# Optimization experiments

Measured on AMD Instinct MI355X. Metric: run time of the kernel, lower is better.

## Reference

```python
import jax, jax.numpy as jnp
from jax import lax
import numpy as np

DIM = 800
FEAT = 192
LAYERS = 5
BLOCK_SZ = [32, 192, 192, 192, 192]
BLOCK_RNG = [0, 32, 224, 416, 608, 800]
HALF = 27  # image_size//4//2 - 1 with image_size=224
EPS = 1e-5


def conv2d(x, w, stride=1, pad=0, groups=1):
    return lax.conv_general_dilated(
        x, w, (stride, stride), [(pad, pad), (pad, pad)],
        dimension_numbers=("NCHW", "OIHW", "NCHW"),
        feature_group_count=groups)


def _bcast(v):
    return v[None, :, None, None]


def setup_inputs() -> dict:
    key = jax.random.key(0)
    ks = jax.random.split(key, 22)
    B = 32
    s = 0.05
    return {
        "x": jax.random.normal(ks[0], (B, 3, 224, 224), jnp.float32),
        "ds_w1": jax.random.normal(ks[1], (16, 3, 3, 3), jnp.float32) * s,
        "ds_b1": jax.random.normal(ks[2], (16,), jnp.float32) * s,
        "bn1_g": jax.random.uniform(ks[3], (16,), jnp.float32) + 0.5,
        "bn1_b": jax.random.normal(ks[4], (16,), jnp.float32) * s,
        "bn1_m": jax.random.normal(ks[5], (16,), jnp.float32) * s,
        "bn1_v": jax.random.uniform(ks[6], (16,), jnp.float32) + 0.5,
        "ds_dw": jax.random.normal(ks[7], (16, 1, 3, 3), jnp.float32) * s,
        "ds_dwb": jax.random.normal(ks[8], (16,), jnp.float32) * s,
        "ds_w2": jax.random.normal(ks[9], (32, 16, 1, 1), jnp.float32) * s,
        "ds_b2": jax.random.normal(ks[10], (32,), jnp.float32) * s,
        "bn2_g": jax.random.uniform(ks[11], (32,), jnp.float32) + 0.5,
        "bn2_b": jax.random.normal(ks[12], (32,), jnp.float32) * s,
        "bn2_m": jax.random.normal(ks[13], (32,), jnp.float32) * s,
        "bn2_v": jax.random.uniform(ks[14], (32,), jnp.float32) + 0.5,
        "conv_dw": jax.random.normal(ks[15], (DIM, 1, 3, 3), jnp.float32) * s,
        "gw": jax.random.normal(ks[16], (DIM, DIM), jnp.float32) * s,
        "in_gamma": jax.random.uniform(ks[17], (DIM,), jnp.float32) + 0.5,
        "in_beta": jax.random.normal(ks[18], (DIM,), jnp.float32) * s,
        "fc_w": jax.random.normal(ks[19], (1000, FEAT), jnp.float32) * s,
        "fc_b": jax.random.normal(ks[20], (1000,), jnp.float32) * s,
    }


def _forward(x, ds_w1, ds_b1, bn1_g, bn1_b, bn1_m, bn1_v, ds_dw, ds_dwb,
             ds_w2, ds_b2, bn2_g, bn2_b, bn2_m, bn2_v, conv_dw, gw,
             in_gamma, in_beta, fc_w, fc_b):
    # ---- downsample stem: conv3x3 s2 -> BN -> ReLU -> dwconv3x3 s2 -> conv1x1 -> BN
    h = conv2d(x, ds_w1, 2, 1) + _bcast(ds_b1)
    h = (h - _bcast(bn1_m)) * _bcast(bn1_g * lax.rsqrt(bn1_v + EPS)) + _bcast(bn1_b)
    h = jax.nn.relu(h)
    h = conv2d(h, ds_dw, 2, 1, groups=16) + _bcast(ds_dwb)
    h = conv2d(h, ds_w2, 1, 0) + _bcast(ds_b2)
    h = (h - _bcast(bn2_m)) * _bcast(bn2_g * lax.rsqrt(bn2_v + EPS)) + _bcast(bn2_b)
    B, _, H, W = h.shape  # (B, 32, 56, 56)
    h = jnp.concatenate([h, jnp.zeros((B, DIM - 32, H, W), h.dtype)], axis=1)

    # ---- per-block InstanceNorm -> ReLU -> depthwise conv -> sliced 1x1 graph conv -> residual
    for i in range(LAYERS):
        s, r0, r1 = BLOCK_SZ[i], BLOCK_RNG[i], BLOCK_RNG[i + 1]
        xa = h[:, :s]
        mu = xa.mean((2, 3), keepdims=True)
        var = ((xa - mu) ** 2).mean((2, 3), keepdims=True)
        xa = (xa - mu) * lax.rsqrt(var + EPS)
        xa = xa * _bcast(in_gamma[r0:r1]) + _bcast(in_beta[r0:r1])
        xa = jax.nn.relu(xa)
        xa = conv2d(xa, conv_dw[r0:r1], 1, 1, groups=s)
        row0 = min(r1, DIM - FEAT)
        xa = jnp.einsum("oc,bchw->bohw", gw[row0:, r0:r1], xa)
        h = (h[:, s:] if i < LAYERS - 1 else h[:, -FEAT:]) + xa

    # ---- AvgPool2d(2) over the 3x3 crop keeps only the top-left 2x2 mean
    out = h[:, :, HALF - 1:HALF + 1, HALF - 1:HALF + 1].mean((2, 3))
    return out @ fc_w.T + fc_b


def reference(x, ds_w1, ds_b1, bn1_g, bn1_b, bn1_m, bn1_v, ds_dw, ds_dwb,
              ds_w2, ds_b2, bn2_g, bn2_b, bn2_m, bn2_v, conv_dw, gw,
              in_gamma, in_beta, fc_w, fc_b):
    return _forward(x, ds_w1, ds_b1, bn1_g, bn1_b, bn1_m, bn1_v, ds_dw, ds_dwb,
                    ds_w2, ds_b2, bn2_g, bn2_b, bn2_m, bn2_v, conv_dw, gw,
                    in_gamma, in_beta, fc_w, fc_b)
```

## Files before the change

### kernel.cpp

```cpp
#include <hip/hip_runtime.h>
#include <stddef.h>

#define EPS 1e-5f
#define N_HW 3136
#define G 32
#define NG (G * N_HW)
#define DIMC 800
#define NTILE 49

typedef unsigned short u16;
typedef __attribute__((ext_vector_type(8))) short short8;
typedef __attribute__((ext_vector_type(4))) float floatx4;

__device__ __forceinline__ u16 f2b(float f) {
  unsigned u = __float_as_uint(f);
  u += 0x7FFFu + ((u >> 16) & 1u);
  return (u16)(u >> 16);
}
__device__ __forceinline__ float blo(unsigned u) { return __uint_as_float(u << 16); }
__device__ __forceinline__ float bhi(unsigned u) { return __uint_as_float(u & 0xFFFF0000u); }

static const size_t XA_OFF  = 0;
static const size_t H0_OFF  = 122028032ull;
static const size_t BLK_OFF = 134873088ull;
static const size_t GWB_OFF = 173408256ull;
static const size_t STS_OFF = 174688256ull;
static const size_t STQ_OFF = 174712832ull;
static const size_t PAT_OFF = 174737408ull;
static const size_t M4_OFF  = 179456000ull;
static const size_t MH_OFF  = M4_OFF + 6144 * 4;
static const size_t OP_OFF  = MH_OFF + 6144 * 4;
static const size_t NEED    = OP_OFF + 6144 * 4;

__global__ __launch_bounds__(256) void gw2bf(const float* __restrict__ gw, u16* __restrict__ gwb) {
  int i = (blockIdx.x * 256 + threadIdx.x) * 4;
  float4 v = *(const float4*)(gw + i);
  gwb[i + 0] = f2b(v.x); gwb[i + 1] = f2b(v.y);
  gwb[i + 2] = f2b(v.z); gwb[i + 3] = f2b(v.w);
}

__global__ __launch_bounds__(256) void zero_stats(float* __restrict__ p) {
  p[blockIdx.x * 256 + threadIdx.x] = 0.f;
}

#define XT_PITCH 226
#define XT_CH (17 * XT_PITCH)
__global__ __launch_bounds__(256) void stem_conv1(
    const float* __restrict__ xg, const float* __restrict__ w, const float* __restrict__ b1,
    const float* __restrict__ g, const float* __restrict__ bb,
    const float* __restrict__ m, const float* __restrict__ v,
    float* __restrict__ h1) {
  __shared__ float xt[3 * XT_CH];
  __shared__ float wt[16 * 27];
  __shared__ float mulc[16], addc[16];
  int blk = blockIdx.x;
  int s = blk % 14;
  int bg = blk / 14;
  int tid = threadIdx.x;

  for (int e = tid; e < 432; e += 256) wt[e] = w[e];
  if (tid < 16) {
    float A = g[tid] * rsqrtf(v[tid] + EPS);
    mulc[tid] = A;
    addc[tid] = (b1[tid] - m[tid]) * A + bb[tid];
  }
  int iy0 = 16 * s - 1;
  for (int e = tid; e < 3 * XT_CH; e += 256) {
    int ci = e / XT_CH;
    int rem = e - ci * XT_CH;
    int r = rem / XT_PITCH;
    int cc = rem - r * XT_PITCH;
    int iy = iy0 + r, ix = cc - 1;
    float val = 0.f;
    if (iy >= 0 && iy < 224 && ix >= 0 && ix < 224)
      val = xg[((size_t)(bg * 3 + ci)) * 224 * 224 + iy * 224 + ix];
    xt[e] = val;
  }
  __syncthreads();

  for (int p = tid; p < 8 * 112; p += 256) {
    int oyl = p / 112, ox = p - oyl * 112;
    float xv[27];
#pragma unroll
    for (int ci = 0; ci < 3; ci++)
#pragma unroll
      for (int ky = 0; ky < 3; ky++)
#pragma unroll
        for (int kx = 0; kx < 3; kx++)
          xv[ci * 9 + ky * 3 + kx] = xt[ci * XT_CH + (2 * oyl + ky) * XT_PITCH + 2 * ox + kx];
    int oy = 8 * s + oyl;
#pragma unroll
    for (int c = 0; c < 16; c++) {
      float acc = 0.f;
#pragma unroll
      for (int t = 0; t < 27; t++) acc += xv[t] * wt[c * 27 + t];
      float y = acc * mulc[c] + addc[c];
      h1[(size_t)(c * G + bg) * 12544 + oy * 112 + ox] = fmaxf(y, 0.f);
    }
  }
}

__global__ __launch_bounds__(256) void stem_dw(
    const float* __restrict__ h1, const float* __restrict__ dw, const float* __restrict__ dwb,
    float* __restrict__ h2) {
  int idx = blockIdx.x * 256 + threadIdx.x;
  int q = idx % N_HW;
  int t = idx / N_HW;
  int bg = t & (G - 1);
  int c = t >> 5;
  int qy = q / 56, qx = q % 56;
  const float* plane = h1 + (size_t)(c * G + bg) * 12544;
  float acc = dwb[c];
#pragma unroll
  for (int ky = 0; ky < 3; ky++) {
    int iy = qy * 2 - 1 + ky;
    if (iy < 0 || iy >= 112) continue;
#pragma unroll
    for (int kx = 0; kx < 3; kx++) {
      int ix = qx * 2 - 1 + kx;
      if (ix < 0 || ix >= 112) continue;
      acc += plane[iy * 112 + ix] * dw[c * 9 + ky * 3 + kx];
    }
  }
  h2[idx] = acc;
}

__global__ __launch_bounds__(256) void stem_pw(
    const float* __restrict__ h2, const float* __restrict__ w2, const float* __restrict__ b2,
    const float* __restrict__ g, const float* __restrict__ bb,
    const float* __restrict__ m, const float* __restrict__ v,
    float* __restrict__ H0) {
  int idx = blockIdx.x * 256 + threadIdx.x;
  int q = idx % N_HW;
  int t = idx / N_HW;
  int bg = t & (G - 1);
  int o = t >> 5;
  float acc = b2[o];
#pragma unroll
  for (int c = 0; c < 16; c++) acc += w2[o * 16 + c] * h2[(size_t)(c * G + bg) * N_HW + q];
  float y = (acc - m[o]) * (g[o] * rsqrtf(v[o] + EPS)) + bb[o];
  H0[idx] = y;
}

template <typename T>
__global__ __launch_bounds__(256) void dw_fused(
    const T* __restrict__ base, const float* __restrict__ cdw,
    const float* __restrict__ in_g, const float* __restrict__ in_b,
    u16* __restrict__ XA, int cdwoff) {
  __shared__ float sm[58 * 58];
  __shared__ float wred[8];
  int blk = blockIdx.x;
  int cl = blk >> 5;
  int c = cdwoff + cl;
  int tid = threadIdx.x;

  if (tid < 58) { sm[tid] = 0.f; sm[57 * 58 + tid] = 0.f; }
  if (tid >= 64 && tid < 120) { int r = tid - 63; sm[r * 58] = 0.f; sm[r * 58 + 57] = 0.f; }

  const T* row = base + (size_t)blk * N_HW;
  float s = 0.f, s2 = 0.f;
  for (int i = tid; i < 392; i += 256) {
    float vals[8];
    if constexpr (sizeof(T) == 2) {
      uint4 u = *(const uint4*)((const u16*)row + i * 8);
      vals[0] = blo(u.x); vals[1] = bhi(u.x);
      vals[2] = blo(u.y); vals[3] = bhi(u.y);
      vals[4] = blo(u.z); vals[5] = bhi(u.z);
      vals[6] = blo(u.w); vals[7] = bhi(u.w);
    } else {
      float4 v0 = *(const float4*)((const float*)row + i * 8);
      float4 v1 = *(const float4*)((const float*)row + i * 8 + 4);
      vals[0] = v0.x; vals[1] = v0.y; vals[2] = v0.z; vals[3] = v0.w;
      vals[4] = v1.x; vals[5] = v1.y; vals[6] = v1.z; vals[7] = v1.w;
    }
    int p = i * 8;
    int y = p / 56, x = p - y * 56;
    float* d = &sm[(y + 1) * 58 + x + 1];
#pragma unroll
    for (int e = 0; e < 8; e++) {
      d[e] = vals[e];
      s += vals[e];
      s2 += vals[e] * vals[e];
    }
  }
#pragma unroll
  for (int o = 32; o > 0; o >>= 1) {
    s += __shfl_down(s, o);
    s2 += __shfl_down(s2, o);
  }
  if ((tid & 63) == 0) { wred[(tid >> 6) * 2] = s; wred[(tid >> 6) * 2 + 1] = s2; }
  __syncthreads();
  float ts = (wred[0] + wred[2]) + (wred[4] + wred[6]);
  float tq = (wred[1] + wred[3]) + (wred[5] + wred[7]);
  float mean = ts * (1.f / N_HW);
  float var = fmaxf(tq * (1.f / N_HW) - mean * mean, 0.f);
  float sc = in_g[c] * rsqrtf(var + EPS);
  float sh = in_b[c] - mean * sc;

  for (int i = tid; i < N_HW; i += 256) {
    int y = i / 56, x = i - y * 56;
    int pos = (y + 1) * 58 + x + 1;
    sm[pos] = fmaxf(sm[pos] * sc + sh, 0.f);
  }
  __syncthreads();

  float w0 = cdw[c * 9 + 0], w1 = cdw[c * 9 + 1], w2 = cdw[c * 9 + 2];
  float w3 = cdw[c * 9 + 3], w4 = cdw[c * 9 + 4], w5 = cdw[c * 9 + 5];
  float w6 = cdw[c * 9 + 6], w7 = cdw[c * 9 + 7], w8 = cdw[c * 9 + 8];
  u16* outp = XA + (size_t)blk * N_HW;
  for (int pp = tid; pp < N_HW / 2; pp += 256) {
    int p = pp * 2;
    int y = p / 56, x = p - y * 56;
    const float* p0 = &sm[y * 58 + x];
    float a0 = p0[0] * w0 + p0[1] * w1 + p0[2] * w2
             + p0[58] * w3 + p0[59] * w4 + p0[60] * w5
             + p0[116] * w6 + p0[117] * w7 + p0[118] * w8;
    float a1 = p0[1] * w0 + p0[2] * w1 + p0[3] * w2
             + p0[59] * w3 + p0[60] * w4 + p0[61] * w5
             + p0[117] * w6 + p0[118] * w7 + p0[119] * w8;
    unsigned pk = (unsigned)f2b(a0) | ((unsigned)f2b(a1) << 16);
    *(unsigned*)&outp[p] = pk;
  }
}

template <int MODE>
__global__ __launch_bounds__(256) void gemm_mfma(
    const u16* __restrict__ A, const u16* __restrict__ B, u16* __restrict__ C,
    float* __restrict__ statS, float* __restrict__ statQ, float* __restrict__ patchf,
    int K) {
  __shared__ u16 As[192][40];
  int n0 = blockIdx.x * 64;
  int tid = threadIdx.x;
  int wave = tid >> 6, lane = tid & 63;
  int wm = wave >> 1, wn = wave & 1;
  int lg = lane >> 4, li = lane & 15;
  floatx4 acc[6][2] = {};

  int ar = tid >> 2, ak = (tid & 3) * 8;
  const u16* Ag = A + (size_t)ar * DIMC + ak;
  const u16* Bg = B + (size_t)(lg * 8) * NG + n0 + wn * 32 + li;

  int nt = K / 32;
  uint4 ra0 = *(const uint4*)(Ag);
  uint4 ra1 = *(const uint4*)(Ag + (size_t)64 * DIMC);
  uint4 ra2 = *(const uint4*)(Ag + (size_t)128 * DIMC);
  short8 bF0, bF1;
#pragma unroll
  for (int e = 0; e < 8; e++) {
    bF0[e] = (short)Bg[(size_t)e * NG];
    bF1[e] = (short)Bg[(size_t)e * NG + 16];
  }

  for (int t = 0; t < nt; t++) {
    *(uint4*)&As[ar][ak]       = ra0;
    *(uint4*)&As[ar + 64][ak]  = ra1;
    *(uint4*)&As[ar + 128][ak] = ra2;
    __syncthreads();
    short8 nb0, nb1;
    bool pf = (t + 1 < nt);
    if (pf) {
      const u16* ag = Ag + (size_t)(t + 1) * 32;
      ra0 = *(const uint4*)(ag);
      ra1 = *(const uint4*)(ag + (size_t)64 * DIMC);
      ra2 = *(const uint4*)(ag + (size_t)128 * DIMC);
      const u16* bg = Bg + (size_t)(t + 1) * 32 * NG;
#pragma unroll
      for (int e = 0; e < 8; e++) {
        nb0[e] = (short)bg[(size_t)e * NG];
        nb1[e] = (short)bg[(size_t)e * NG + 16];
      }
    }
    short8 aF[6];
#pragma unroll
    for (int mi = 0; mi < 6; mi++)
      aF[mi] = *(const short8*)&As[wm * 96 + mi * 16 + li][lg * 8];
#pragma unroll
    for (int mi = 0; mi < 6; mi++) {
      acc[mi][0] = __builtin_amdgcn_mfma_f32_16x16x32_bf16(aF[mi], bF0, acc[mi][0], 0, 0, 0);
      acc[mi][1] = __builtin_amdgcn_mfma_f32_16x16x32_bf16(aF[mi], bF1, acc[mi][1], 0, 0, 0);
    }
    __syncthreads();
    if (pf) { bF0 = nb0; bF1 = nb1; }
  }

  if constexpr (MODE == 0) {
#pragma unroll
    for (int mi = 0; mi < 6; mi++) {
#pragma unroll
      for (int ni = 0; ni < 2; ni++) {
        int row = wm * 96 + mi * 16 + lg * 4;
        int col = n0 + wn * 32 + ni * 16 + li;
        u16* cp = C + (size_t)row * NG + col;
#pragma unroll
        for (int r = 0; r < 4; r++) cp[(size_t)r * NG] = f2b(acc[mi][ni][r]);
      }
    }
  } else {
    int bg = blockIdx.x / NTILE;
    int tile = blockIdx.x % NTILE;
#pragma unroll
    for (int mi = 0; mi < 6; mi++) {
#pragma unroll
      for (int r = 0; r < 4; r++) {
        float v0 = acc[mi][0][r], v1 = acc[mi][1][r];
        float s = v0 + v1;
        float q = v0 * v0 + v1 * v1;
#pragma unroll
        for (int msk = 1; msk < 16; msk <<= 1) {
          s += __shfl_xor(s, msk);
          q += __shfl_xor(q, msk);
        }
        if (li == 0) {
          int row = wm * 96 + mi * 16 + lg * 4 + r;
          atomicAdd(&statS[row * 32 + bg], s);
          atomicAdd(&statQ[row * 32 + bg], q);
        }
      }
    }
    if (tile >= 22 && tile <= 24) {
#pragma unroll
      for (int mi = 0; mi < 6; mi++) {
#pragma unroll
        for (int ni = 0; ni < 2; ni++) {
          int row = wm * 96 + mi * 16 + lg * 4;
          int pc = (tile - 22) * 64 + wn * 32 + ni * 16 + li;
#pragma unroll
          for (int r = 0; r < 4; r++)
            patchf[((size_t)(row + r) * 32 + bg) * 192 + pc] = acc[mi][ni][r];
        }
      }
    }
  }
}

__global__ __launch_bounds__(256) void head_m4(
    const float* __restrict__ statS, const float* __restrict__ statQ,
    const float* __restrict__ patchf,
    const float* __restrict__ in_g, const float* __restrict__ in_b,
    const float* __restrict__ cdw, float* __restrict__ m4, float* __restrict__ meanH) {
  int idx = blockIdx.x * 256 + threadIdx.x;
  if (idx >= 192 * 32) return;
  int cl = idx >> 5;
  int c = 608 + cl;
  float mean = statS[idx] * (1.f / N_HW);
  float var = fmaxf(statQ[idx] * (1.f / N_HW) - mean * mean, 0.f);
  float sc = in_g[c] * rsqrtf(var + EPS);
  float sh = in_b[c] - mean * sc;
  const float* pf = patchf + (size_t)idx * 192;
  float val[4][4];
#pragma unroll
  for (int dy = 0; dy < 4; dy++)
#pragma unroll
    for (int dx = 0; dx < 4; dx++) {
      int hw = (25 + dy) * 56 + 25 + dx;
      float v = pf[((hw >> 6) - 22) * 64 + (hw & 63)];
      val[dy][dx] = fmaxf(v * sc + sh, 0.f);
    }
  const float* w = cdw + c * 9;
  float acc = 0.f;
#pragma unroll
  for (int oy = 1; oy < 3; oy++)
#pragma unroll
    for (int ox = 1; ox < 3; ox++)
#pragma unroll
      for (int ky = 0; ky < 3; ky++)
#pragma unroll
        for (int kx = 0; kx < 3; kx++)
          acc += val[oy + ky - 1][ox + kx - 1] * w[ky * 3 + kx];
  m4[idx] = acc * 0.25f;
  float mh = 0.f;
#pragma unroll
  for (int dy = 0; dy < 2; dy++)
#pragma unroll
    for (int dx = 0; dx < 2; dx++) {
      int hw = (26 + dy) * 56 + 26 + dx;
      mh += pf[((hw >> 6) - 22) * 64 + (hw & 63)];
    }
  meanH[idx] = mh * 0.25f;
}

__global__ __launch_bounds__(256) void head_mix(
    const float* __restrict__ gw, const float* __restrict__ m4, const float* __restrict__ meanH,
    float* __restrict__ out_pre) {
  int idx = blockIdx.x * 256 + threadIdx.x;
  if (idx >= G * 192) return;
  int j = idx % 192;
  int bg = idx / 192;
  float acc = meanH[j * G + bg];
  const float* grow = gw + (size_t)(608 + j) * DIMC + 608;
  for (int c = 0; c < 192; c++) acc += grow[c] * m4[c * G + bg];
  out_pre[idx] = acc;
}

__global__ __launch_bounds__(256) void head_fc(
    const float* __restrict__ out_pre, const float* __restrict__ fc_w,
    const float* __restrict__ fc_b, float* __restrict__ outg) {
  int idx = blockIdx.x * 256 + threadIdx.x;
  if (idx >= G * 1000) return;
  int t = idx % 1000;
  int bg = idx / 1000;
  float acc = fc_b[t];
  const float* wr = fc_w + (size_t)t * 192;
  const float* hr = out_pre + (size_t)bg * 192;
  for (int j = 0; j < 192; j++) acc += wr[j] * hr[j];
  outg[idx] = acc;
}

extern "C" void kernel_launch(void* const* d_in, const int* in_sizes, int n_in,
                              void* d_out, int out_size, void* d_ws, size_t ws_size,
                              hipStream_t stream) {
  const float* x      = (const float*)d_in[0];
  const float* ds_w1  = (const float*)d_in[1];
  const float* ds_b1  = (const float*)d_in[2];
  const float* bn1_g  = (const float*)d_in[3];
  const float* bn1_b  = (const float*)d_in[4];
  const float* bn1_m  = (const float*)d_in[5];
  const float* bn1_v  = (const float*)d_in[6];
  const float* ds_dw  = (const float*)d_in[7];
  const float* ds_dwb = (const float*)d_in[8];
  const float* ds_w2  = (const float*)d_in[9];
  const float* ds_b2  = (const float*)d_in[10];
  const float* bn2_g  = (const float*)d_in[11];
  const float* bn2_b  = (const float*)d_in[12];
  const float* bn2_m  = (const float*)d_in[13];
  const float* bn2_v  = (const float*)d_in[14];
  const float* cdw    = (const float*)d_in[15];
  const float* gw     = (const float*)d_in[16];
  const float* in_g   = (const float*)d_in[17];
  const float* in_b   = (const float*)d_in[18];
  const float* fc_w   = (const float*)d_in[19];
  const float* fc_b   = (const float*)d_in[20];
  float* out = (float*)d_out;
  char* ws = (char*)d_ws;

  if (ws_size < NEED) return;

  u16*   XAc    = (u16*)(ws + XA_OFF);
  float* H0     = (float*)(ws + H0_OFF);
  u16*   blockb = (u16*)(ws + BLK_OFF);
  u16*   gwb    = (u16*)(ws + GWB_OFF);
  float* statS  = (float*)(ws + STS_OFF);
  float* statQ  = (float*)(ws + STQ_OFF);
  float* patchf = (float*)(ws + PAT_OFF);
  float* m4     = (float*)(ws + M4_OFF);
  float* meanH  = (float*)(ws + MH_OFF);
  float* opre   = (float*)(ws + OP_OFF);
  float* h1     = (float*)(ws + BLK_OFF);
  float* h2     = h1 + (size_t)16 * G * 12544;

  gw2bf<<<625, 256, 0, stream>>>(gw, gwb);
  zero_stats<<<48, 256, 0, stream>>>(statS);

  static const int CDWOFF[4] = {0, 32, 224, 416};
  static const int SZ[4]     = {32, 192, 192, 192};
  static const int RA[4]     = {32, 224, 416, 608};
  static const int KK[4]     = {32, 224, 416, 608};

  stem_conv1<<<14 * G, 256, 0, stream>>>(
      x, ds_w1, ds_b1, bn1_g, bn1_b, bn1_m, bn1_v, h1);
  stem_dw<<<16 * G * N_HW / 256, 256, 0, stream>>>(h1, ds_dw, ds_dwb, h2);
  stem_pw<<<32 * G * N_HW / 256, 256, 0, stream>>>(
      h2, ds_w2, ds_b2, bn2_g, bn2_b, bn2_m, bn2_v, H0);

  for (int i = 0; i < 4; i++) {
    if (i == 0)
      dw_fused<float><<<SZ[i] * G, 256, 0, stream>>>(
          H0, cdw, in_g, in_b, XAc + (size_t)CDWOFF[i] * NG, CDWOFF[i]);
    else
      dw_fused<u16><<<SZ[i] * G, 256, 0, stream>>>(
          blockb, cdw, in_g, in_b, XAc + (size_t)CDWOFF[i] * NG, CDWOFF[i]);
    if (i < 3)
      gemm_mfma<0><<<NG / 64, 256, 0, stream>>>(
          gwb + (size_t)RA[i] * DIMC, XAc, blockb, nullptr, nullptr, nullptr, KK[i]);
    else
      gemm_mfma<1><<<NG / 64, 256, 0, stream>>>(
          gwb + (size_t)RA[i] * DIMC, XAc, nullptr, statS, statQ, patchf, KK[i]);
  }

  head_m4<<<24, 256, 0, stream>>>(statS, statQ, patchf, in_g, in_b, cdw, m4, meanH);
  head_mix<<<(G * 192 + 255) / 256, 256, 0, stream>>>(gw, m4, meanH, opre);
  head_fc<<<(G * 1000 + 255) / 256, 256, 0, stream>>>(opre, fc_w, fc_b, out);
}
```

Baseline: 431.5 us.

## Store depthwise output in K-tiled layout and fuse instance-norm stats into producers

The depthwise kernel now writes its bf16 output in a K-tiled layout (32 channels contiguous per pixel), so the GEMM can load B fragments with two 16-byte loads instead of eight strided scalar loads. Instance-norm statistics are now accumulated with atomics in the producing kernels (stem pointwise and every GEMM epilogue). This lets the depthwise kernel work on 4-row strips across 32 channels instead of staging a full plane per channel. The head patch is also shrunk to the 4x4 pixels it needs. The cost is more atomics in every GEMM epilogue and a strided transposed store pattern in the depthwise kernel.

Result: slower. 699.6 us (+62.1%).

```diff
diff --git a/kernel.cpp b/kernel.cpp
--- a/kernel.cpp
+++ b/kernel.cpp
@@ -20,17 +20,16 @@
 __device__ __forceinline__ float blo(unsigned u) { return __uint_as_float(u << 16); }
 __device__ __forceinline__ float bhi(unsigned u) { return __uint_as_float(u & 0xFFFF0000u); }
 
-static const size_t XA_OFF  = 0;
-static const size_t H0_OFF  = 122028032ull;
-static const size_t BLK_OFF = 134873088ull;
-static const size_t GWB_OFF = 173408256ull;
-static const size_t STS_OFF = 174688256ull;
-static const size_t STQ_OFF = 174712832ull;
-static const size_t PAT_OFF = 174737408ull;
-static const size_t M4_OFF  = 179456000ull;
-static const size_t MH_OFF  = M4_OFF + 6144 * 4;
-static const size_t OP_OFF  = MH_OFF + 6144 * 4;
-static const size_t NEED    = OP_OFF + 6144 * 4;
+static const size_t XAKT_OFF = 0;
+static const size_t BUF1_OFF = 122028032ull;
+static const size_t H0F_OFF  = 160563200ull;
+static const size_t GWB_OFF  = 173408256ull;
+static const size_t STAT_OFF = 174688256ull;
+static const size_t P16_OFF  = 174934016ull;
+static const size_t M4_OFF   = 175327232ull;
+static const size_t MH_OFF   = M4_OFF + 6144 * 4;
+static const size_t OP_OFF   = MH_OFF + 6144 * 4;
+static const size_t NEED     = OP_OFF + 6144 * 4;
 
 __global__ __launch_bounds__(256) void gw2bf(const float* __restrict__ gw, u16* __restrict__ gwb) {
   int i = (blockIdx.x * 256 + threadIdx.x) * 4;
@@ -125,109 +124,136 @@
   h2[idx] = acc;
 }
 
-__global__ __launch_bounds__(256) void stem_pw(
+__global__ __launch_bounds__(256) void stem_pw_v2(
     const float* __restrict__ h2, const float* __restrict__ w2, const float* __restrict__ b2,
     const float* __restrict__ g, const float* __restrict__ bb,
     const float* __restrict__ m, const float* __restrict__ v,
-    float* __restrict__ H0) {
-  int idx = blockIdx.x * 256 + threadIdx.x;
-  int q = idx % N_HW;
-  int t = idx / N_HW;
-  int bg = t & (G - 1);
-  int o = t >> 5;
-  float acc = b2[o];
-#pragma unroll
-  for (int c = 0; c < 16; c++) acc += w2[o * 16 + c] * h2[(size_t)(c * G + bg) * N_HW + q];
-  float y = (acc - m[o]) * (g[o] * rsqrtf(v[o] + EPS)) + bb[o];
-  H0[idx] = y;
+    float* __restrict__ H0, float* __restrict__ stat0) {
+  int r = blockIdx.x;
+  int o = r >> 5, bg = r & 31;
+  int tid = threadIdx.x;
+  float w[16];
+#pragma unroll
+  for (int c = 0; c < 16; c++) w[c] = w2[o * 16 + c];
+  float A = g[o] * rsqrtf(v[o] + EPS);
+  float mul = A, add = bb[o] - m[o] * A;
+  const float* h2r = h2 + (size_t)bg * N_HW;
+  float* outp = H0 + (size_t)r * N_HW;
+  float s = 0.f, s2 = 0.f;
+  for (int q = tid; q < N_HW; q += 256) {
+    float acc = b2[o];
+#pragma unroll
+    for (int c = 0; c < 16; c++) acc += w[c] * h2r[(size_t)c * G * N_HW + q];
+    float y = acc * mul + add;
+    outp[q] = y;
+    s += y; s2 += y * y;
+  }
+#pragma unroll
+  for (int o2 = 32; o2 > 0; o2 >>= 1) {
+    s += __shfl_down(s, o2);
+    s2 += __shfl_down(s2, o2);
+  }
+  if ((tid & 63) == 0) {
+    atomicAdd(&stat0[r], s);
+    atomicAdd(&stat0[6144 + r], s2);
+  }
 }
 
 template <typename T>
-__global__ __launch_bounds__(256) void dw_fused(
-    const T* __restrict__ base, const float* __restrict__ cdw,
+__global__ __launch_bounds__(256) void dw_kt(
+    const T* __restrict__ in, const float* __restrict__ cdw,
     const float* __restrict__ in_g, const float* __restrict__ in_b,
-    u16* __restrict__ XA, int cdwoff) {
-  __shared__ float sm[58 * 58];
-  __shared__ float wred[8];
+    const float* __restrict__ stat, u16* __restrict__ XAkt,
+    int cdwoff, int ngroups) {
+  __shared__ float sm[32 * 350];
+  __shared__ float ssc[32], ssh[32], swt[32 * 9];
   int blk = blockIdx.x;
-  int cl = blk >> 5;
-  int c = cdwoff + cl;
+  int grp = blk % ngroups;
+  int t2 = blk / ngroups;
+  int strip = t2 % 14;
+  int bg = t2 / 14;
   int tid = threadIdx.x;
-
-  if (tid < 58) { sm[tid] = 0.f; sm[57 * 58 + tid] = 0.f; }
-  if (tid >= 64 && tid < 120) { int r = tid - 63; sm[r * 58] = 0.f; sm[r * 58 + 57] = 0.f; }
-
-  const T* row = base + (size_t)blk * N_HW;
-  float s = 0.f, s2 = 0.f;
-  for (int i = tid; i < 392; i += 256) {
-    float vals[8];
-    if constexpr (sizeof(T) == 2) {
-      uint4 u = *(const uint4*)((const u16*)row + i * 8);
-      vals[0] = blo(u.x); vals[1] = bhi(u.x);
-      vals[2] = blo(u.y); vals[3] = bhi(u.y);
-      vals[4] = blo(u.z); vals[5] = bhi(u.z);
-      vals[6] = blo(u.w); vals[7] = bhi(u.w);
+  if (tid < 32) {
+    int cl = grp * 32 + tid;
+    int c = cdwoff + cl;
+    int sidx = cl * 32 + bg;
+    float S = stat[sidx], Q = stat[6144 + sidx];
+    float mean = S * (1.f / N_HW);
+    float var = fmaxf(Q * (1.f / N_HW) - mean * mean, 0.f);
+    float sc = in_g[c] * rsqrtf(var + EPS);
+    ssc[tid] = sc;
+    ssh[tid] = in_b[c] - mean * sc;
+  }
+  for (int e = tid; e < 288; e += 256)
+    swt[e] = cdw[(size_t)(cdwoff + grp * 32) * 9 + e];
+  __syncthreads();
+
+  int y0 = strip * 4;
+  if (tid < 192) {
+    int ch = tid / 6, rr = tid % 6;
+    int y = y0 - 1 + rr;
+    float* dst = &sm[ch * 350 + rr * 58];
+    if (y < 0 || y > 55) {
+#pragma unroll
+      for (int x = 0; x < 58; x++) dst[x] = 0.f;
     } else {
-      float4 v0 = *(const float4*)((const float*)row + i * 8);
-      float4 v1 = *(const float4*)((const float*)row + i * 8 + 4);
-      vals[0] = v0.x; vals[1] = v0.y; vals[2] = v0.z; vals[3] = v0.w;
-      vals[4] = v1.x; vals[5] = v1.y; vals[6] = v1.z; vals[7] = v1.w;
-    }
-    int p = i * 8;
-    int y = p / 56, x = p - y * 56;
-    float* d = &sm[(y + 1) * 58 + x + 1];
-#pragma unroll
-    for (int e = 0; e < 8; e++) {
-      d[e] = vals[e];
-      s += vals[e];
-      s2 += vals[e] * vals[e];
-    }
-  }
-#pragma unroll
-  for (int o = 32; o > 0; o >>= 1) {
-    s += __shfl_down(s, o);
-    s2 += __shfl_down(s2, o);
-  }
-  if ((tid & 63) == 0) { wred[(tid >> 6) * 2] = s; wred[(tid >> 6) * 2 + 1] = s2; }
+      float sc = ssc[ch], sh = ssh[ch];
+      dst[0] = 0.f; dst[57] = 0.f;
+      const T* src = in + ((size_t)(grp * 32 + ch) * G + bg) * N_HW + y * 56;
+      if constexpr (sizeof(T) == 2) {
+#pragma unroll
+        for (int xx = 0; xx < 7; xx++) {
+          uint4 u = *(const uint4*)((const u16*)src + xx * 8);
+          float* d = dst + 1 + xx * 8;
+          d[0] = fmaxf(blo(u.x) * sc + sh, 0.f);
+          d[1] = fmaxf(bhi(u.x) * sc + sh, 0.f);
+          d[2] = fmaxf(blo(u.y) * sc + sh, 0.f);
+          d[3] = fmaxf(bhi(u.y) * sc + sh, 0.f);
+          d[4] = fmaxf(blo(u.z) * sc + sh, 0.f);
+          d[5] = fmaxf(bhi(u.z) * sc + sh, 0.f);
+          d[6] = fmaxf(blo(u.w) * sc + sh, 0.f);
+          d[7] = fmaxf(bhi(u.w) * sc + sh, 0.f);
+        }
+      } else {
+#pragma unroll
+        for (int xx = 0; xx < 14; xx++) {
+          float4 vv = *(const float4*)((const float*)src + xx * 4);
+          float* d = dst + 1 + xx * 4;
+          d[0] = fmaxf(vv.x * sc + sh, 0.f);
+          d[1] = fmaxf(vv.y * sc + sh, 0.f);
+          d[2] = fmaxf(vv.z * sc + sh, 0.f);
+          d[3] = fmaxf(vv.w * sc + sh, 0.f);
+        }
+      }
+    }
+  }
   __syncthreads();
-  float ts = (wred[0] + wred[2]) + (wred[4] + wred[6]);
-  float tq = (wred[1] + wred[3]) + (wred[5] + wred[7]);
-  float mean = ts * (1.f / N_HW);
-  float var = fmaxf(tq * (1.f / N_HW) - mean * mean, 0.f);
-  float sc = in_g[c] * rsqrtf(var + EPS);
-  float sh = in_b[c] - mean * sc;
-
-  for (int i = tid; i < N_HW; i += 256) {
-    int y = i / 56, x = i - y * 56;
-    int pos = (y + 1) * 58 + x + 1;
-    sm[pos] = fmaxf(sm[pos] * sc + sh, 0.f);
-  }
-  __syncthreads();
-
-  float w0 = cdw[c * 9 + 0], w1 = cdw[c * 9 + 1], w2 = cdw[c * 9 + 2];
-  float w3 = cdw[c * 9 + 3], w4 = cdw[c * 9 + 4], w5 = cdw[c * 9 + 5];
-  float w6 = cdw[c * 9 + 6], w7 = cdw[c * 9 + 7], w8 = cdw[c * 9 + 8];
-  u16* outp = XA + (size_t)blk * N_HW;
-  for (int pp = tid; pp < N_HW / 2; pp += 256) {
-    int p = pp * 2;
-    int y = p / 56, x = p - y * 56;
-    const float* p0 = &sm[y * 58 + x];
-    float a0 = p0[0] * w0 + p0[1] * w1 + p0[2] * w2
-             + p0[58] * w3 + p0[59] * w4 + p0[60] * w5
-             + p0[116] * w6 + p0[117] * w7 + p0[118] * w8;
-    float a1 = p0[1] * w0 + p0[2] * w1 + p0[3] * w2
-             + p0[59] * w3 + p0[60] * w4 + p0[61] * w5
-             + p0[117] * w6 + p0[118] * w7 + p0[119] * w8;
-    unsigned pk = (unsigned)f2b(a0) | ((unsigned)f2b(a1) << 16);
-    *(unsigned*)&outp[p] = pk;
+
+  size_t tilebase = ((size_t)(cdwoff >> 5) + grp) * NG;
+  for (int e = tid; e < 896; e += 256) {
+    int pos = e >> 2, k8 = e & 3;
+    int ry = pos / 56, x = pos % 56;
+    int y = y0 + ry;
+    u16 outv[8];
+#pragma unroll
+    for (int j = 0; j < 8; j++) {
+      int ch = k8 * 8 + j;
+      const float* b = &sm[ch * 350 + ry * 58 + x];
+      const float* w = &swt[ch * 9];
+      float a = b[0] * w[0] + b[1] * w[1] + b[2] * w[2]
+              + b[58] * w[3] + b[59] * w[4] + b[60] * w[5]
+              + b[116] * w[6] + b[117] * w[7] + b[118] * w[8];
+      outv[j] = f2b(a);
+    }
+    *(uint4*)(XAkt + (tilebase + (size_t)bg * N_HW + y * 56 + x) * 32 + k8 * 8) =
+        *(const uint4*)outv;
   }
 }
 
 template <int MODE>
-__global__ __launch_bounds__(256) void gemm_mfma(
-    const u16* __restrict__ A, const u16* __restrict__ B, u16* __restrict__ C,
-    float* __restrict__ statS, float* __restrict__ statQ, float* __restrict__ patchf,
-    int K) {
+__global__ __launch_bounds__(256) void gemm_v2(
+    const u16* __restrict__ A, const u16* __restrict__ Bkt, u16* __restrict__ C,
+    float* __restrict__ stat, float* __restrict__ p16, int K) {
   __shared__ u16 As[192][40];
   int n0 = blockIdx.x * 64;
   int tid = threadIdx.x;
@@ -238,51 +264,66 @@
 
   int ar = tid >> 2, ak = (tid & 3) * 8;
   const u16* Ag = A + (size_t)ar * DIMC + ak;
-  const u16* Bg = B + (size_t)(lg * 8) * NG + n0 + wn * 32 + li;
+  const u16* Bg = Bkt + ((size_t)(n0 + wn * 32 + li)) * 32 + lg * 8;
 
   int nt = K / 32;
   uint4 ra0 = *(const uint4*)(Ag);
   uint4 ra1 = *(const uint4*)(Ag + (size_t)64 * DIMC);
   uint4 ra2 = *(const uint4*)(Ag + (size_t)128 * DIMC);
-  short8 bF0, bF1;
-#pragma unroll
-  for (int e = 0; e < 8; e++) {
-    bF0[e] = (short)Bg[(size_t)e * NG];
-    bF1[e] = (short)Bg[(size_t)e * NG + 16];
-  }
+  uint4 rb0 = *(const uint4*)(Bg);
+  uint4 rb1 = *(const uint4*)(Bg + 512);
 
   for (int t = 0; t < nt; t++) {
     *(uint4*)&As[ar][ak]       = ra0;
     *(uint4*)&As[ar + 64][ak]  = ra1;
     *(uint4*)&As[ar + 128][ak] = ra2;
     __syncthreads();
-    short8 nb0, nb1;
+    uint4 nb0, nb1;
     bool pf = (t + 1 < nt);
     if (pf) {
       const u16* ag = Ag + (size_t)(t + 1) * 32;
       ra0 = *(const uint4*)(ag);
       ra1 = *(const uint4*)(ag + (size_t)64 * DIMC);
       ra2 = *(const uint4*)(ag + (size_t)128 * DIMC);
-      const u16* bg = Bg + (size_t)(t + 1) * 32 * NG;
-#pragma unroll
-      for (int e = 0; e < 8; e++) {
-        nb0[e] = (short)bg[(size_t)e * NG];
-        nb1[e] = (short)bg[(size_t)e * NG + 16];
-      }
+      const u16* bgp = Bg + (size_t)(t + 1) * NG * 32;
+      nb0 = *(const uint4*)(bgp);
+      nb1 = *(const uint4*)(bgp + 512);
     }
     short8 aF[6];
 #pragma unroll
     for (int mi = 0; mi < 6; mi++)
       aF[mi] = *(const short8*)&As[wm * 96 + mi * 16 + li][lg * 8];
+    short8 bF0 = *(short8*)&rb0;
+    short8 bF1 = *(short8*)&rb1;
 #pragma unroll
     for (int mi = 0; mi < 6; mi++) {
       acc[mi][0] = __builtin_amdgcn_mfma_f32_16x16x32_bf16(aF[mi], bF0, acc[mi][0], 0, 0, 0);
       acc[mi][1] = __builtin_amdgcn_mfma_f32_16x16x32_bf16(aF[mi], bF1, acc[mi][1], 0, 0, 0);
     }
     __syncthreads();
-    if (pf) { bF0 = nb0; bF1 = nb1; }
-  }
-
+    if (pf) { rb0 = nb0; rb1 = nb1; }
+  }
+
+  int bg = blockIdx.x / NTILE;
+#pragma unroll
+  for (int mi = 0; mi < 6; mi++) {
+#pragma unroll
+    for (int r = 0; r < 4; r++) {
+      float v0 = acc[mi][0][r], v1 = acc[mi][1][r];
+      float s = v0 + v1;
+      float q = v0 * v0 + v1 * v1;
+#pragma unroll
+      for (int msk = 1; msk < 16; msk <<= 1) {
+        s += __shfl_xor(s, msk);
+        q += __shfl_xor(q, msk);
+      }
+      if (li == 0) {
+        int row = wm * 96 + mi * 16 + lg * 4 + r;
+        atomicAdd(&stat[row * 32 + bg], s);
+        atomicAdd(&stat[6144 + row * 32 + bg], q);
+      }
+    }
+  }
   if constexpr (MODE == 0) {
 #pragma unroll
     for (int mi = 0; mi < 6; mi++) {
@@ -296,66 +337,45 @@
       }
     }
   } else {
-    int bg = blockIdx.x / NTILE;
-    int tile = blockIdx.x % NTILE;
-#pragma unroll
-    for (int mi = 0; mi < 6; mi++) {
-#pragma unroll
-      for (int r = 0; r < 4; r++) {
-        float v0 = acc[mi][0][r], v1 = acc[mi][1][r];
-        float s = v0 + v1;
-        float q = v0 * v0 + v1 * v1;
-#pragma unroll
-        for (int msk = 1; msk < 16; msk <<= 1) {
-          s += __shfl_xor(s, msk);
-          q += __shfl_xor(q, msk);
-        }
-        if (li == 0) {
-          int row = wm * 96 + mi * 16 + lg * 4 + r;
-          atomicAdd(&statS[row * 32 + bg], s);
-          atomicAdd(&statQ[row * 32 + bg], q);
-        }
+#pragma unroll
+    for (int ni = 0; ni < 2; ni++) {
+      int col = n0 + wn * 32 + ni * 16 + li;
+      int hw = col % 3136;
+      int yy = hw / 56, xx = hw % 56;
+      int dy = yy - 25, dx = xx - 25;
+      if ((unsigned)dy < 4u && (unsigned)dx < 4u) {
+#pragma unroll
+        for (int mi = 0; mi < 6; mi++)
+#pragma unroll
+          for (int r = 0; r < 4; r++) {
+            int row = wm * 96 + mi * 16 + lg * 4 + r;
+            p16[((size_t)row * 32 + bg) * 16 + dy * 4 + dx] = acc[mi][ni][r];
+          }
       }
     }
-    if (tile >= 22 && tile <= 24) {
-#pragma unroll
-      for (int mi = 0; mi < 6; mi++) {
-#pragma unroll
-        for (int ni = 0; ni < 2; ni++) {
-          int row = wm * 96 + mi * 16 + lg * 4;
-          int pc = (tile - 22) * 64 + wn * 32 + ni * 16 + li;
-#pragma unroll
-          for (int r = 0; r < 4; r++)
-            patchf[((size_t)(row + r) * 32 + bg) * 192 + pc] = acc[mi][ni][r];
-        }
-      }
-    }
   }
 }
 
 __global__ __launch_bounds__(256) void head_m4(
-    const float* __restrict__ statS, const float* __restrict__ statQ,
-    const float* __restrict__ patchf,
+    const float* __restrict__ stat4, const float* __restrict__ p16,
     const float* __restrict__ in_g, const float* __restrict__ in_b,
     const float* __restrict__ cdw, float* __restrict__ m4, float* __restrict__ meanH) {
   int idx = blockIdx.x * 256 + threadIdx.x;
   if (idx >= 192 * 32) return;
   int cl = idx >> 5;
   int c = 608 + cl;
-  float mean = statS[idx] * (1.f / N_HW);
-  float var = fmaxf(statQ[idx] * (1.f / N_HW) - mean * mean, 0.f);
+  float S = stat4[idx], Q = stat4[6144 + idx];
+  float mean = S * (1.f / N_HW);
+  float var = fmaxf(Q * (1.f / N_HW) - mean * mean, 0.f);
   float sc = in_g[c] * rsqrtf(var + EPS);
   float sh = in_b[c] - mean * sc;
-  const float* pf = patchf + (size_t)idx * 192;
+  const float* pf = p16 + (size_t)idx * 16;
   float val[4][4];
 #pragma unroll
   for (int dy = 0; dy < 4; dy++)
 #pragma unroll
-    for (int dx = 0; dx < 4; dx++) {
-      int hw = (25 + dy) * 56 + 25 + dx;
-      float v = pf[((hw >> 6) - 22) * 64 + (hw & 63)];
-      val[dy][dx] = fmaxf(v * sc + sh, 0.f);
-    }
+    for (int dx = 0; dx < 4; dx++)
+      val[dy][dx] = fmaxf(pf[dy * 4 + dx] * sc + sh, 0.f);
   const float* w = cdw + c * 9;
   float acc = 0.f;
 #pragma unroll
@@ -368,15 +388,7 @@
         for (int kx = 0; kx < 3; kx++)
           acc += val[oy + ky - 1][ox + kx - 1] * w[ky * 3 + kx];
   m4[idx] = acc * 0.25f;
-  float mh = 0.f;
-#pragma unroll
-  for (int dy = 0; dy < 2; dy++)
-#pragma unroll
-    for (int dx = 0; dx < 2; dx++) {
-      int hw = (26 + dy) * 56 + 26 + dx;
-      mh += pf[((hw >> 6) - 22) * 64 + (hw & 63)];
-    }
-  meanH[idx] = mh * 0.25f;
+  meanH[idx] = 0.25f * (pf[5] + pf[6] + pf[9] + pf[10]);
 }
 
 __global__ __launch_bounds__(256) void head_mix(
@@ -435,49 +447,50 @@
 
   if (ws_size < NEED) return;
 
-  u16*   XAc    = (u16*)(ws + XA_OFF);
-  float* H0     = (float*)(ws + H0_OFF);
-  u16*   blockb = (u16*)(ws + BLK_OFF);
-  u16*   gwb    = (u16*)(ws + GWB_OFF);
-  float* statS  = (float*)(ws + STS_OFF);
-  float* statQ  = (float*)(ws + STQ_OFF);
-  float* patchf = (float*)(ws + PAT_OFF);
-  float* m4     = (float*)(ws + M4_OFF);
-  float* meanH  = (float*)(ws + MH_OFF);
-  float* opre   = (float*)(ws + OP_OFF);
-  float* h1     = (float*)(ws + BLK_OFF);
-  float* h2     = h1 + (size_t)16 * G * 12544;
+  u16*   XAkt  = (u16*)(ws + XAKT_OFF);
+  u16*   buf1  = (u16*)(ws + BUF1_OFF);
+  float* H0f   = (float*)(ws + H0F_OFF);
+  u16*   gwb   = (u16*)(ws + GWB_OFF);
+  float* stats = (float*)(ws + STAT_OFF);
+  float* p16   = (float*)(ws + P16_OFF);
+  float* m4    = (float*)(ws + M4_OFF);
+  float* meanH = (float*)(ws + MH_OFF);
+  float* opre  = (float*)(ws + OP_OFF);
+  float* h1    = (float*)buf1;
+  float* h2    = h1 + (size_t)16 * G * 12544;
 
   gw2bf<<<625, 256, 0, stream>>>(gw, gwb);
-  zero_stats<<<48, 256, 0, stream>>>(statS);
+  zero_stats<<<240, 256, 0, stream>>>(stats);
 
   static const int CDWOFF[4] = {0, 32, 224, 416};
-  static const int SZ[4]     = {32, 192, 192, 192};
+  static const int NGRP[4]   = {1, 6, 6, 6};
   static const int RA[4]     = {32, 224, 416, 608};
   static const int KK[4]     = {32, 224, 416, 608};
 
   stem_conv1<<<14 * G, 256, 0, stream>>>(
       x, ds_w1, ds_b1, bn1_g, bn1_b, bn1_m, bn1_v, h1);
   stem_dw<<<16 * G * N_HW / 256, 256, 0, stream>>>(h1, ds_dw, ds_dwb, h2);
-  stem_pw<<<32 * G * N_HW / 256, 256, 0, stream>>>(
-      h2, ds_w2, ds_b2, bn2_g, bn2_b, bn2_m, bn2_v, H0);
+  stem_pw_v2<<<1024, 256, 0, stream>>>(
+      h2, ds_w2, ds_b2, bn2_g, bn2_b, bn2_m, bn2_v, H0f, stats );
 
   for (int i = 0; i < 4; i++) {
+    float* statIn  = stats + (size_t)i * 12288;
+    float* statOut = stats + (size_t)(i + 1) * 12288;
     if (i == 0)
-      dw_fused<float><<<SZ[i] * G, 256, 0, stream>>>(
-          H0, cdw, in_g, in_b, XAc + (size_t)CDWOFF[i] * NG, CDWOFF[i]);
+      dw_kt<float><<<32 * 14 * NGRP[i], 256, 0, stream>>>(
+          H0f, cdw, in_g, in_b, statIn, XAkt, CDWOFF[i], NGRP[i]);
     else
-      dw_fused<u16><<<SZ[i] * G, 256, 0, stream>>>(
-          blockb, cdw, in_g, in_b, XAc + (size_t)CDWOFF[i] * NG, CDWOFF[i]);
+      dw_kt<u16><<<32 * 14 * NGRP[i], 256, 0, stream>>>(
+          buf1, cdw, in_g, in_b, statIn, XAkt, CDWOFF[i], NGRP[i]);
     if (i < 3)
-      gemm_mfma<0><<<NG / 64, 256, 0, stream>>>(
-          gwb + (size_t)RA[i] * DIMC, XAc, blockb, nullptr, nullptr, nullptr, KK[i]);
+      gemm_v2<0><<<NG / 64, 256, 0, stream>>>(
+          gwb + (size_t)RA[i] * DIMC, XAkt, buf1, statOut, nullptr, KK[i]);
     else
-      gemm_mfma<1><<<NG / 64, 256, 0, stream>>>(
-          gwb + (size_t)RA[i] * DIMC, XAc, nullptr, statS, statQ, patchf, KK[i]);
-  }
-
-  head_m4<<<24, 256, 0, stream>>>(statS, statQ, patchf, in_g, in_b, cdw, m4, meanH);
+      gemm_v2<1><<<NG / 64, 256, 0, stream>>>(
+          gwb + (size_t)RA[i] * DIMC, XAkt, nullptr, statOut, p16, KK[i]);
+  }
+
+  head_m4<<<24, 256, 0, stream>>>(stats + 4 * 12288, p16, in_g, in_b, cdw, m4, meanH);
   head_mix<<<(G * 192 + 255) / 256, 256, 0, stream>>>(gw, m4, meanH, opre);
   head_fc<<<(G * 1000 + 255) / 256, 256, 0, stream>>>(opre, fc_w, fc_b, out);
 }
```
